# Kernel tuning notes

Hardware: AMD Instinct MI355X
Metric: run time of the kernel (lower is better)

## Reference

```python
import jax, jax.numpy as jnp
import numpy as np

E4M3_MAX = 448.0
BLOCK = 128


def _quant_dequant(x, block=BLOCK):
    # x: [R, C] -> block-wise fake-quantized [R, C]
    R, C = x.shape
    pad_r = (-R) % block
    pad_c = (-C) % block
    xp = jnp.pad(x, ((0, pad_r), (0, pad_c)))
    Rp, Cp = R + pad_r, C + pad_c
    # [nR, block, nC, block] -> [nR, nC, block, block]
    xb = xp.reshape(Rp // block, block, Cp // block, block).transpose(0, 2, 1, 3)
    amax = jnp.max(jnp.abs(xb), axis=(-1, -2), keepdims=True)
    scale = jnp.maximum(amax / E4M3_MAX, 1e-8)
    xq = jnp.clip(jnp.round(xb / scale), -E4M3_MAX, E4M3_MAX)
    xdq = (xq * scale).transpose(0, 2, 1, 3).reshape(Rp, Cp)
    return xdq[:R, :C]


def setup_inputs() -> dict:
    key = jax.random.key(0)
    k1, k2 = jax.random.split(key)
    B, S, D_in, D_out = 4, 2048, 4096, 4096
    x = jax.random.normal(k1, (B, S, D_in), dtype=jnp.float32)
    weight = jax.random.normal(k2, (D_out, D_in), dtype=jnp.float32)
    bias = jnp.zeros((D_out,), dtype=jnp.float32)
    return {"x": x, "weight": weight, "bias": bias}


def reference(x, weight, bias):
    batch_shape = x.shape[:-1]
    in_features = x.shape[-1]
    x_flat = x.reshape(-1, in_features)
    x_dq = _quant_dequant(x_flat)
    w_dq = _quant_dequant(weight)
    out = x_dq @ w_dq.T + bias  # [N, out_features]
    return out.reshape(*batch_shape, weight.shape[0])
```

## Files before the change

kernel.cpp:

```cpp
#include <hip/hip_runtime.h>
#include <hip/hip_fp16.h>
#include <stdint.h>

typedef _Float16 half_t;
typedef half_t half8 __attribute__((ext_vector_type(8)));
typedef float f32x4 __attribute__((ext_vector_type(4)));
typedef float f32x16 __attribute__((ext_vector_type(16)));

#define E4M3_MAX 448.0f
#define MFMA32 __builtin_amdgcn_mfma_f32_32x32x16_f16

constexpr int Mdim = 8192, Ndim = 4096, Kdim = 4096;
constexpr int NKT = Kdim / 64;
constexpr int NITER = NKT / 2;
constexpr int NTN = Ndim / 256;
constexpr int NTM = Mdim / 256;
constexpr int LDS_BYTES = 131072;

__global__ __launch_bounds__(256) void quant_kernel(const float* __restrict__ in,
                                                    half_t* __restrict__ outq,
                                                    int C) {
    const int cb = blockIdx.x, rb = blockIdx.y;
    const int tid = threadIdx.x;
    const int col4 = tid & 31;
    const int rsub = tid >> 5;

    const float* base = in + (size_t)(rb * 128 + rsub) * C + cb * 128 + col4 * 4;

    f32x4 v[16];
    float amax = 0.0f;
#pragma unroll
    for (int p = 0; p < 16; ++p) {
        v[p] = *(const f32x4*)(base + (size_t)p * 8 * C);
        amax = fmaxf(amax, fmaxf(fmaxf(fabsf(v[p].x), fabsf(v[p].y)),
                                 fmaxf(fabsf(v[p].z), fabsf(v[p].w))));
    }
#pragma unroll
    for (int off = 32; off > 0; off >>= 1)
        amax = fmaxf(amax, __shfl_xor(amax, off, 64));
    __shared__ float red[4];
    if ((tid & 63) == 0) red[tid >> 6] = amax;
    __syncthreads();
    amax = fmaxf(fmaxf(red[0], red[1]), fmaxf(red[2], red[3]));

    const float scale = fmaxf(amax / E4M3_MAX, 1e-8f);
    const float rs = 1.0f / scale;

    half_t* obase = outq + (size_t)(rb * 128 + rsub) * C + cb * 128 + col4 * 4;
#pragma unroll
    for (int p = 0; p < 16; ++p) {
        float q0 = fminf(fmaxf(rintf(v[p].x * rs), -E4M3_MAX), E4M3_MAX) * scale;
        float q1 = fminf(fmaxf(rintf(v[p].y * rs), -E4M3_MAX), E4M3_MAX) * scale;
        float q2 = fminf(fmaxf(rintf(v[p].z * rs), -E4M3_MAX), E4M3_MAX) * scale;
        float q3 = fminf(fmaxf(rintf(v[p].w * rs), -E4M3_MAX), E4M3_MAX) * scale;
        union { half_t h[4]; uint64_t u; } pk;
        pk.h[0] = (half_t)q0; pk.h[1] = (half_t)q1;
        pk.h[2] = (half_t)q2; pk.h[3] = (half_t)q3;
        *(uint64_t*)(obase + (size_t)p * 8 * C) = pk.u;
    }
}

__device__ __forceinline__ void async16(const half_t* g, char* l) {
    __builtin_amdgcn_global_load_lds((const __attribute__((address_space(1))) void*)g,
                                     (__attribute__((address_space(3))) void*)l, 16, 0, 0);
}

extern __shared__ char smem[];

__global__ __launch_bounds__(512, 2) void gemm_kernel(
    const half_t* __restrict__ A, const half_t* __restrict__ B,
    const float* __restrict__ bias, float* __restrict__ C) {

    const int tid = threadIdx.x;
    const int lane = tid & 63;
    const int wid = tid >> 6;
    const int l31 = lane & 31;
    const int kh  = lane >> 5;
    const int r7  = l31 & 7;
    const int wr = wid >> 2;
    const int wc = wid & 3;

    const int bid = blockIdx.x;
    constexpr int cpx = (NTM * NTN) / 8;
    const int id = (bid & 7) * cpx + (bid >> 3);
    const int tm = id / NTN, tn = id % NTN;

    const int r0 = tid >> 3;
    const int ks = ((tid & 7) ^ (r0 & 7)) * 8;
    const half_t* Abase = A + (size_t)(tm * 256 + r0) * Kdim + ks;
    const half_t* Bbase = B + (size_t)(tn * 256 + r0) * Kdim + ks;
    char* ldstA = smem + tid * 16;
    char* ldstB = smem + 65536 + tid * 16;

#define STG_AS(b, s, kt)                                                                  \
    async16(Abase + (size_t)((s) * 64) * Kdim + (kt) * 64,                                \
            ldstA + (b) * 32768 + (s) * 8192)
#define STG_B(b, h, kt) do {                                                              \
    async16(Bbase + (size_t)((h) * 128) * Kdim + (kt) * 64,                               \
            ldstB + (b) * 32768 + (h) * 16384);                                           \
    async16(Bbase + (size_t)((h) * 128 + 64) * Kdim + (kt) * 64,                          \
            ldstB + (b) * 32768 + (h) * 16384 + 8192); } while (0)

    STG_B(0, 0, 0); STG_B(0, 1, 0);
    STG_AS(0, 0, 0); STG_AS(0, 1, 0); STG_AS(0, 2, 0); STG_AS(0, 3, 0);
    STG_B(1, 0, 1); STG_B(1, 1, 1);
    asm volatile("s_waitcnt vmcnt(4)" ::: "memory");
    __builtin_amdgcn_sched_barrier(0);
    __builtin_amdgcn_s_barrier();
    __builtin_amdgcn_sched_barrier(0);

    const int kbit = (kh ^ (r7 & 1)) << 4;
    const int sx = r7 >> 1;
    int sof[4];
    sof[0] = (0 ^ sx) << 5; sof[1] = (1 ^ sx) << 5;
    sof[2] = (2 ^ sx) << 5; sof[3] = (3 ^ sx) << 5;
    const char* pA = smem + wr * 16384 + l31 * 128 + kbit;
    const char* pB = smem + 65536 + wc * 8192 + l31 * 128 + kbit;

    f32x16 acc[4][2] = {};
    half8 bfr[2][4];

#define BARSEQ                                                                            \
    __builtin_amdgcn_sched_barrier(0);                                                    \
    __builtin_amdgcn_s_barrier();                                                         \
    __builtin_amdgcn_sched_barrier(0);

#define LDA32(b, q)                                                                       \
    half8 aa0 = *(const half8*)(pA + (b)*32768 + ((q)>>1)*8192 + ((q)&1)*4096 + sof[0]);  \
    half8 aa1 = *(const half8*)(pA + (b)*32768 + ((q)>>1)*8192 + ((q)&1)*4096 + sof[1]);  \
    half8 aa2 = *(const half8*)(pA + (b)*32768 + ((q)>>1)*8192 + ((q)&1)*4096 + sof[2]);  \
    half8 aa3 = *(const half8*)(pA + (b)*32768 + ((q)>>1)*8192 + ((q)&1)*4096 + sof[3]);

#define LDB32(b)                                                                          \
    bfr[0][0] = *(const half8*)(pB + (b)*32768 + 0*4096 + sof[0]);                        \
    bfr[0][1] = *(const half8*)(pB + (b)*32768 + 0*4096 + sof[1]);                        \
    bfr[0][2] = *(const half8*)(pB + (b)*32768 + 0*4096 + sof[2]);                        \
    bfr[0][3] = *(const half8*)(pB + (b)*32768 + 0*4096 + sof[3]);                        \
    bfr[1][0] = *(const half8*)(pB + (b)*32768 + 1*4096 + sof[0]);                        \
    bfr[1][1] = *(const half8*)(pB + (b)*32768 + 1*4096 + sof[1]);                        \
    bfr[1][2] = *(const half8*)(pB + (b)*32768 + 1*4096 + sof[2]);                        \
    bfr[1][3] = *(const half8*)(pB + (b)*32768 + 1*4096 + sof[3]);

#define MFMAQ32(q)                                                                        \
    __builtin_amdgcn_s_setprio(1);                                                        \
    acc[q][0] = MFMA32(aa0, bfr[0][0], acc[q][0], 0, 0, 0);                               \
    acc[q][1] = MFMA32(aa0, bfr[1][0], acc[q][1], 0, 0, 0);                               \
    acc[q][0] = MFMA32(aa1, bfr[0][1], acc[q][0], 0, 0, 0);                               \
    acc[q][1] = MFMA32(aa1, bfr[1][1], acc[q][1], 0, 0, 0);                               \
    acc[q][0] = MFMA32(aa2, bfr[0][2], acc[q][0], 0, 0, 0);                               \
    acc[q][1] = MFMA32(aa2, bfr[1][2], acc[q][1], 0, 0, 0);                               \
    acc[q][0] = MFMA32(aa3, bfr[0][3], acc[q][0], 0, 0, 0);                               \
    acc[q][1] = MFMA32(aa3, bfr[1][3], acc[q][1], 0, 0, 0);                               \
    __builtin_amdgcn_s_setprio(0);

    for (int i = 0; i < NITER; ++i) {
        const int kA1  = 2 * i + 1;
        const int ktn0 = (2 * i + 2) & (NKT - 1);
        const int ktn1 = (2 * i + 3) & (NKT - 1);

        {
            LDB32(0)
            LDA32(0, 0)
            STG_AS(1, 0, kA1); STG_AS(1, 2, kA1);
            BARSEQ
            MFMAQ32(0)
        }
        {
            LDA32(0, 1)
            STG_AS(1, 1, kA1); STG_AS(1, 3, kA1);
            BARSEQ
            MFMAQ32(1)
        }
        {
            LDA32(0, 2)
            STG_B(0, 0, ktn0);
            BARSEQ
            MFMAQ32(2)
        }
        {
            LDA32(0, 3)
            STG_B(0, 1, ktn0);
            asm volatile("s_waitcnt vmcnt(4)" ::: "memory");
            BARSEQ
            MFMAQ32(3)
        }
        {
            LDB32(1)
            LDA32(1, 0)
            STG_AS(0, 0, ktn0); STG_AS(0, 2, ktn0);
            BARSEQ
            MFMAQ32(0)
        }
        {
            LDA32(1, 1)
            STG_AS(0, 1, ktn0); STG_AS(0, 3, ktn0);
            BARSEQ
            MFMAQ32(1)
        }
        {
            LDA32(1, 2)
            STG_B(1, 0, ktn1);
            BARSEQ
            MFMAQ32(2)
        }
        {
            LDA32(1, 3)
            STG_B(1, 1, ktn1);
            asm volatile("s_waitcnt vmcnt(4)" ::: "memory");
            BARSEQ
            MFMAQ32(3)
        }
    }

    asm volatile("s_waitcnt vmcnt(0)" ::: "memory");

    const int rbase = tm * 256 + wr * 128 + 4 * kh;
    const int cb = tn * 256 + wc * 64 + l31;
    const float bv0 = bias[cb];
    const float bv1 = bias[cb + 32];
#pragma unroll
    for (int q = 0; q < 4; ++q) {
#pragma unroll
        for (int r = 0; r < 16; ++r) {
            const int row = rbase + q * 32 + (r & 3) + 8 * (r >> 2);
            float* p = C + (size_t)row * Ndim + cb;
            p[0]  = acc[q][0][r] + bv0;
            p[32] = acc[q][1][r] + bv1;
        }
    }
}

extern "C" void kernel_launch(void* const* d_in, const int* in_sizes, int n_in,
                              void* d_out, int out_size, void* d_ws, size_t ws_size,
                              hipStream_t stream) {
    const float* x = (const float*)d_in[0];
    const float* w = (const float*)d_in[1];
    const float* bias = (const float*)d_in[2];
    float* out = (float*)d_out;

    if (in_sizes[2] != Ndim || in_sizes[1] != Ndim * Kdim || in_sizes[0] != Mdim * Kdim)
        return;

    const size_t xq_bytes = (size_t)Mdim * Kdim * sizeof(half_t);
    const size_t wq_bytes = (size_t)Ndim * Kdim * sizeof(half_t);
    if (ws_size < xq_bytes + wq_bytes) return;

    half_t* xq = (half_t*)d_ws;
    half_t* wq = (half_t*)((char*)d_ws + xq_bytes);

    quant_kernel<<<dim3(Kdim / 128, Mdim / 128), 256, 0, stream>>>(x, xq, Kdim);
    quant_kernel<<<dim3(Kdim / 128, Ndim / 128), 256, 0, stream>>>(w, wq, Kdim);

    (void)hipFuncSetAttribute((const void*)gemm_kernel,
                              hipFuncAttributeMaxDynamicSharedMemorySize, LDS_BYTES);

    gemm_kernel<<<dim3(NTM * NTN), dim3(512), LDS_BYTES, stream>>>(xq, wq, bias, out);
}
```

Measured before the change: 311.2 us.

## Replace XOR-swizzled LDS layout with MFMA-fragment-ordered staging layout

Changes how global A/B tiles are laid out in LDS: instead of row-major rows with an XOR swizzle, each thread's 16-byte global load lands where an MFMA lane will later read it contiguously (lane*16). The intent is to remove swizzle offset arithmetic and bank conflicts on LDS reads, making fragment reads linear. In exchange, global loads become less coalesced (each thread reads 16B chunks at strided rows with narrower per-row spans), which may hurt global memory efficiency.

```diff
diff --git a/kernel.cpp b/kernel.cpp
--- a/kernel.cpp
+++ b/kernel.cpp
@@ -76,7 +76,6 @@
     const int wid = tid >> 6;
     const int l31 = lane & 31;
     const int kh  = lane >> 5;
-    const int r7  = l31 & 7;
     const int wr = wid >> 2;
     const int wc = wid & 3;
 
@@ -85,21 +84,20 @@
     const int id = (bid & 7) * cpx + (bid >> 3);
     const int tm = id / NTN, tn = id % NTN;
 
-    const int r0 = tid >> 3;
-    const int ks = ((tid & 7) ^ (r0 & 7)) * 8;
-    const half_t* Abase = A + (size_t)(tm * 256 + r0) * Kdim + ks;
-    const half_t* Bbase = B + (size_t)(tn * 256 + r0) * Kdim + ks;
+    const int sA_row = ((tid >> 6) & 1) * 32 + (tid & 31);
+    const int sA_ch  = (tid >> 7) * 2 + ((tid >> 5) & 1);
+    const half_t* AbaseG = A + (size_t)(tm * 256 + sA_row) * Kdim + sA_ch * 8;
+    const int sB_row = (tid >> 6) * 32 + (tid & 31);
+    const half_t* BbaseG = B + (size_t)(tn * 256 + sB_row) * Kdim + ((tid >> 5) & 1) * 8;
     char* ldstA = smem + tid * 16;
     char* ldstB = smem + 65536 + tid * 16;
 
-#define STG_AS(b, s, kt)                                                                  \
-    async16(Abase + (size_t)((s) * 64) * Kdim + (kt) * 64,                                \
-            ldstA + (b) * 32768 + (s) * 8192)
-#define STG_B(b, h, kt) do {                                                              \
-    async16(Bbase + (size_t)((h) * 128) * Kdim + (kt) * 64,                               \
-            ldstB + (b) * 32768 + (h) * 16384);                                           \
-    async16(Bbase + (size_t)((h) * 128 + 64) * Kdim + (kt) * 64,                          \
-            ldstB + (b) * 32768 + (h) * 16384 + 8192); } while (0)
+#define STG_AS(b, sl, kt)                                                                 \
+    async16(AbaseG + (size_t)((sl) * 64) * Kdim + (kt) * 64,                              \
+            ldstA + (b) * 32768 + (sl) * 8192)
+#define STG_B1(b, s, kt)                                                                  \
+    async16(BbaseG + (kt) * 64 + (s) * 16, ldstB + (b) * 32768 + (s) * 8192)
+#define STG_B(b, h, kt) do { STG_B1(b, 2*(h), kt); STG_B1(b, 2*(h)+1, kt); } while (0)
 
     STG_B(0, 0, 0); STG_B(0, 1, 0);
     STG_AS(0, 0, 0); STG_AS(0, 1, 0); STG_AS(0, 2, 0); STG_AS(0, 3, 0);
@@ -109,13 +107,8 @@
     __builtin_amdgcn_s_barrier();
     __builtin_amdgcn_sched_barrier(0);
 
-    const int kbit = (kh ^ (r7 & 1)) << 4;
-    const int sx = r7 >> 1;
-    int sof[4];
-    sof[0] = (0 ^ sx) << 5; sof[1] = (1 ^ sx) << 5;
-    sof[2] = (2 ^ sx) << 5; sof[3] = (3 ^ sx) << 5;
-    const char* pA = smem + wr * 16384 + l31 * 128 + kbit;
-    const char* pB = smem + 65536 + wc * 8192 + l31 * 128 + kbit;
+    const char* pA = smem + wr * 16384 + lane * 16;
+    const char* pB = smem + 65536 + wc * 2048 + lane * 16;
 
     f32x16 acc[4][2] = {};
     half8 bfr[2][4];
@@ -126,20 +119,20 @@
     __builtin_amdgcn_sched_barrier(0);
 
 #define LDA32(b, q)                                                                       \
-    half8 aa0 = *(const half8*)(pA + (b)*32768 + ((q)>>1)*8192 + ((q)&1)*4096 + sof[0]);  \
-    half8 aa1 = *(const half8*)(pA + (b)*32768 + ((q)>>1)*8192 + ((q)&1)*4096 + sof[1]);  \
-    half8 aa2 = *(const half8*)(pA + (b)*32768 + ((q)>>1)*8192 + ((q)&1)*4096 + sof[2]);  \
-    half8 aa3 = *(const half8*)(pA + (b)*32768 + ((q)>>1)*8192 + ((q)&1)*4096 + sof[3]);
+    half8 aa0 = *(const half8*)(pA + (b)*32768 + ((q)>>1)*8192 + ((q)&1)*1024 + 0*2048);  \
+    half8 aa1 = *(const half8*)(pA + (b)*32768 + ((q)>>1)*8192 + ((q)&1)*1024 + 1*2048);  \
+    half8 aa2 = *(const half8*)(pA + (b)*32768 + ((q)>>1)*8192 + ((q)&1)*1024 + 2*2048);  \
+    half8 aa3 = *(const half8*)(pA + (b)*32768 + ((q)>>1)*8192 + ((q)&1)*1024 + 3*2048);
 
 #define LDB32(b)                                                                          \
-    bfr[0][0] = *(const half8*)(pB + (b)*32768 + 0*4096 + sof[0]);                        \
-    bfr[0][1] = *(const half8*)(pB + (b)*32768 + 0*4096 + sof[1]);                        \
-    bfr[0][2] = *(const half8*)(pB + (b)*32768 + 0*4096 + sof[2]);                        \
-    bfr[0][3] = *(const half8*)(pB + (b)*32768 + 0*4096 + sof[3]);                        \
-    bfr[1][0] = *(const half8*)(pB + (b)*32768 + 1*4096 + sof[0]);                        \
-    bfr[1][1] = *(const half8*)(pB + (b)*32768 + 1*4096 + sof[1]);                        \
-    bfr[1][2] = *(const half8*)(pB + (b)*32768 + 1*4096 + sof[2]);                        \
-    bfr[1][3] = *(const half8*)(pB + (b)*32768 + 1*4096 + sof[3]);
+    bfr[0][0] = *(const half8*)(pB + (b)*32768 + 0*8192 + 0*1024);                        \
+    bfr[0][1] = *(const half8*)(pB + (b)*32768 + 1*8192 + 0*1024);                        \
+    bfr[0][2] = *(const half8*)(pB + (b)*32768 + 2*8192 + 0*1024);                        \
+    bfr[0][3] = *(const half8*)(pB + (b)*32768 + 3*8192 + 0*1024);                        \
+    bfr[1][0] = *(const half8*)(pB + (b)*32768 + 0*8192 + 1*1024);                        \
+    bfr[1][1] = *(const half8*)(pB + (b)*32768 + 1*8192 + 1*1024);                        \
+    bfr[1][2] = *(const half8*)(pB + (b)*32768 + 2*8192 + 1*1024);                        \
+    bfr[1][3] = *(const half8*)(pB + (b)*32768 + 3*8192 + 1*1024);
 
 #define MFMAQ32(q)                                                                        \
     __builtin_amdgcn_s_setprio(1);                                                        \
```

Result: slower. 341.8 us (+9.8%).
